# Performance work log

Hardware: AMD Instinct MI355X
Metric: run time of the kernel (lower is better)

The kernel has to match this reference:

```python
import jax, jax.numpy as jnp
import numpy as np

N_STUDENT = 100000
N_COURSE = 20000
N_EDGES = 1000000
HIDDEN = 128


def setup_inputs() -> dict:
    key = jax.random.key(0)
    ks = jax.random.split(key, 8)
    scale = 1.0 / np.sqrt(2 * HIDDEN)
    return {
        "z_student": jax.random.normal(ks[0], (N_STUDENT, HIDDEN), dtype=jnp.float32),
        "z_course": jax.random.normal(ks[1], (N_COURSE, HIDDEN), dtype=jnp.float32),
        "row": jax.random.randint(ks[2], (N_EDGES,), 0, N_STUDENT, dtype=jnp.int64),
        "col": jax.random.randint(ks[3], (N_EDGES,), 0, N_COURSE, dtype=jnp.int64),
        "W1": jax.random.normal(ks[4], (2 * HIDDEN, HIDDEN), dtype=jnp.float32) * scale,
        "b1": jnp.zeros((HIDDEN,), dtype=jnp.float32),
        "W2": jax.random.normal(ks[5], (HIDDEN, 1), dtype=jnp.float32) * (1.0 / np.sqrt(HIDDEN)),
        "b2": jnp.zeros((1,), dtype=jnp.float32),
    }


def reference(z_student, z_course, row, col, W1, b1, W2, b2):
    # gather endpoint embeddings and concat along feature dim: [E, 2H]
    z = jnp.concatenate([z_student[row], z_course[col]], axis=-1)
    h = jax.nn.relu(z @ W1 + b1)   # [E, H]
    out = h @ W2 + b2              # [E, 1]
    return out.reshape(-1)
```

## Files before the change

kernel.cpp:

```cpp
#include <hip/hip_runtime.h>
#include <hip/hip_bf16.h>
#include <hip/hip_fp16.h>


typedef _Float16 half2v __attribute__((ext_vector_type(2)));
typedef _Float16 half8v __attribute__((ext_vector_type(8)));
typedef __fp16   fp16x2 __attribute__((ext_vector_type(2)));
typedef float    float4v __attribute__((ext_vector_type(4)));

__global__ __launch_bounds__(256) void conv_w(const float* __restrict__ W1,
                                              const float* __restrict__ W2,
                                              _Float16* __restrict__ Wt,
                                              _Float16* __restrict__ w2h) {
    int b = blockIdx.x, t = threadIdx.x;
    if (b == 8) { if (t < 128) w2h[t] = (_Float16)W2[t]; return; }
    __shared__ _Float16 lds[32][136];
    int h = b >> 2, n0 = (b & 3) * 32;
    for (int i = 0; i < 16; ++i) {
        int idx = i * 256 + t;
        int k = idx >> 5, nn = idx & 31;
        lds[nn][k] = (_Float16)W1[(h * 128 + k) * 128 + n0 + nn];
    }
    __syncthreads();
    for (int j = 0; j < 2; ++j) {
        int idx = j * 256 + t;
        int nn = idx >> 4, kc = idx & 15;
        half8v v;
        #pragma unroll
        for (int q = 0; q < 8; ++q) v[q] = lds[nn][kc * 8 + q];
        *(half8v*)&Wt[((h * 128 + n0 + nn) * 128) + kc * 8] = v;
    }
}

__global__ __launch_bounds__(256) void gemm_u(
    const float* __restrict__ Zs, const float* __restrict__ Zc,
    const _Float16* __restrict__ Wt, const float* __restrict__ b1,
    _Float16* __restrict__ Us, _Float16* __restrict__ Uc,
    int Ms, int Mc, int nbs)
{
    __shared__ uint4 ldsW[2048];
    const int bid = blockIdx.x, t = threadIdx.x;

    const float* Z; _Float16* U; const _Float16* W; int M, m0, addB;
    if (bid < nbs) { Z = Zs; U = Us; M = Ms; m0 = bid * 64;         W = Wt;         addB = 1; }
    else           { Z = Zc; U = Uc; M = Mc; m0 = (bid - nbs) * 64; W = Wt + 16384; addB = 0; }

    const uint4* Wv = (const uint4*)W;
    #pragma unroll
    for (int i = 0; i < 8; ++i) {
        int j = i * 256 + t;
        int n = j >> 4, ch = j & 15;
        ldsW[n * 16 + (ch ^ ((n >> 3) & 7))] = Wv[j];
    }
    __syncthreads();

    const int wave = t >> 6, lane = t & 63, quad = lane >> 4, l16 = lane & 15;
    int mrow = m0 + wave * 16 + l16;
    int mload = mrow < M ? mrow : M - 1;
    const float* zrow = Z + (long)mload * 128;

    float4v acc[8];
    #pragma unroll
    for (int nt = 0; nt < 8; ++nt) acc[nt] = (float4v)(0.0f);

    #pragma unroll
    for (int c = 0; c < 4; ++c) {
        const float4v* pa = (const float4v*)(zrow + c * 32 + quad * 8);
        float4v a0 = pa[0], a1 = pa[1];
        fp16x2 p[4];
        p[0] = __builtin_amdgcn_cvt_pkrtz(a0[0], a0[1]);
        p[1] = __builtin_amdgcn_cvt_pkrtz(a0[2], a0[3]);
        p[2] = __builtin_amdgcn_cvt_pkrtz(a1[0], a1[1]);
        p[3] = __builtin_amdgcn_cvt_pkrtz(a1[2], a1[3]);
        half8v af;
        __builtin_memcpy(&af, &p[0], 16);
        const int ch = c * 4 + quad;
        #pragma unroll
        for (int nt = 0; nt < 8; ++nt) {
            const int n = l16 * 8 + nt;
            const half8v* pb = (const half8v*)&ldsW[n * 16 + (ch ^ (l16 & 7))];
            acc[nt] = __builtin_amdgcn_mfma_f32_16x16x32_f16(af, *pb, acc[nt], 0, 0, 0);
        }
    }

    float bv[8];
    if (addB) {
        const float4v* pb1 = (const float4v*)(b1 + l16 * 8);
        float4v x0 = pb1[0], x1 = pb1[1];
        bv[0]=x0[0]; bv[1]=x0[1]; bv[2]=x0[2]; bv[3]=x0[3];
        bv[4]=x1[0]; bv[5]=x1[1]; bv[6]=x1[2]; bv[7]=x1[3];
    } else {
        #pragma unroll
        for (int i = 0; i < 8; ++i) bv[i] = 0.0f;
    }

    const int rbase = m0 + wave * 16 + quad * 4;
    #pragma unroll
    for (int r = 0; r < 4; ++r) {
        int rr = rbase + r;
        if (rr < M) {
            half8v o;
            #pragma unroll
            for (int nt = 0; nt < 8; ++nt) o[nt] = (_Float16)(acc[nt][r] + bv[nt]);
            *(half8v*)&U[(long)rr * 128 + l16 * 8] = o;
        }
    }
}

__global__ __launch_bounds__(256) void edge_kernel(
    const int* __restrict__ row, const int* __restrict__ col,
    const _Float16* __restrict__ us, const _Float16* __restrict__ uc,
    const _Float16* __restrict__ w2h, const float* __restrict__ b2,
    float* __restrict__ out, int E)
{
    const int t = threadIdx.x;
    const int sub = t & 7;
    long e = (long)blockIdx.x * 32 + (t >> 3);
    if (e >= E) return;
    int r = row[e], c = col[e];

    const uint4* pa = (const uint4*)(us  + (long)r * 128 + sub * 16);
    const uint4* pb = (const uint4*)(uc  + (long)c * 128 + sub * 16);
    const uint4* pw = (const uint4*)(w2h + sub * 16);
    uint4 a0 = pa[0], a1 = pa[1];
    uint4 c0 = pb[0], c1 = pb[1];
    uint4 w0 = pw[0], w1 = pw[1];

    half2v A[8], B[8], W[8];
    *(uint4*)&A[0] = a0; *(uint4*)&A[4] = a1;
    *(uint4*)&B[0] = c0; *(uint4*)&B[4] = c1;
    *(uint4*)&W[0] = w0; *(uint4*)&W[4] = w1;

    const half2v zero = {(_Float16)0, (_Float16)0};
    float s = 0.0f;
    #pragma unroll
    for (int i = 0; i < 8; ++i) {
        half2v h = A[i] + B[i];
        h = __builtin_elementwise_max(h, zero);
        s += (float)h[0] * (float)W[i][0];
        s += (float)h[1] * (float)W[i][1];
    }
    s += __shfl_xor(s, 1);
    s += __shfl_xor(s, 2);
    s += __shfl_xor(s, 4);
    if (sub == 0) out[e] = s + b2[0];
}

extern "C" void kernel_launch(void* const* d_in, const int* in_sizes, int n_in,
                              void* d_out, int out_size, void* d_ws, size_t ws_size,
                              hipStream_t stream) {
    const float* zs  = (const float*)d_in[0];
    const float* zc  = (const float*)d_in[1];
    const int*   row = (const int*)d_in[2];
    const int*   col = (const int*)d_in[3];
    const float* W1  = (const float*)d_in[4];
    const float* b1  = (const float*)d_in[5];
    const float* W2  = (const float*)d_in[6];
    const float* b2  = (const float*)d_in[7];
    float* out = (float*)d_out;

    const int Ms = in_sizes[0] / 128;
    const int Mc = in_sizes[1] / 128;
    const int E  = in_sizes[2];

    _Float16* Wt  = (_Float16*)d_ws;
    _Float16* w2h = (_Float16*)((char*)d_ws + 65536);
    _Float16* us  = (_Float16*)((char*)d_ws + 65536 + 256);
    _Float16* uc  = us + (size_t)Ms * 128;

    const int nbs = (Ms + 63) / 64, nbc = (Mc + 63) / 64;

    conv_w<<<9, 256, 0, stream>>>(W1, W2, Wt, w2h);
    gemm_u<<<nbs + nbc, 256, 0, stream>>>(zs, zc, Wt, b1, us, uc, Ms, Mc, nbs);
    edge_kernel<<<(E + 31) / 32, 256, 0, stream>>>(row, col, us, uc, w2h, b2, out, E);
}
```

Measured before the change: 169.6 us.

## Bucket edges by student row and XCD to improve gather cache locality

Adds a histogram, scan and scatter pass that groups edges into 256 buckets keyed on row>>9, with buckets interleaved so each of 8 block groups handles a contiguous row range. The edge kernel then walks these permuted edges in persistent blocks, so each group's student-embedding gathers stay within a smaller working set that can sit in a local L2. This targets cache misses on the 25 MB fp16 student table, at the cost of three extra kernels, atomics, an 8 MB permutation buffer and scattered output writes. It also assumes col < 32768 and row < 131072 so both fit in one 32-bit packed key.

```diff
diff --git a/kernel.cpp b/kernel.cpp
--- a/kernel.cpp
+++ b/kernel.cpp
@@ -8,12 +8,26 @@
 typedef __fp16   fp16x2 __attribute__((ext_vector_type(2)));
 typedef float    float4v __attribute__((ext_vector_type(4)));
 
+#define NB 256
+#define EBLK 2048
+#define B8 128
+
+static __device__ __forceinline__ int sort_key(int r) {
+    int key = r >> 9;
+    return (key & 7) * 32 + (key >> 3);
+}
+
 __global__ __launch_bounds__(256) void conv_w(const float* __restrict__ W1,
                                               const float* __restrict__ W2,
                                               _Float16* __restrict__ Wt,
-                                              _Float16* __restrict__ w2h) {
+                                              _Float16* __restrict__ w2h,
+                                              unsigned* __restrict__ hist) {
     int b = blockIdx.x, t = threadIdx.x;
-    if (b == 8) { if (t < 128) w2h[t] = (_Float16)W2[t]; return; }
+    if (b == 8) {
+        if (t < 128) w2h[t] = (_Float16)W2[t];
+        hist[t] = 0u;
+        return;
+    }
     __shared__ _Float16 lds[32][136];
     int h = b >> 2, n0 = (b & 3) * 32;
     for (int i = 0; i < 16; ++i) {
@@ -29,6 +43,78 @@
         #pragma unroll
         for (int q = 0; q < 8; ++q) v[q] = lds[nn][kc * 8 + q];
         *(half8v*)&Wt[((h * 128 + n0 + nn) * 128) + kc * 8] = v;
+    }
+}
+
+__global__ __launch_bounds__(256) void hist_k(const int* __restrict__ row,
+                                              unsigned* __restrict__ hist, int E) {
+    __shared__ unsigned h[NB];
+    int t = threadIdx.x;
+    h[t] = 0;
+    __syncthreads();
+    int b0 = blockIdx.x * EBLK;
+    #pragma unroll
+    for (int i = 0; i < 8; ++i) {
+        int e = b0 + i * 256 + t;
+        if (e < E) atomicAdd(&h[sort_key(row[e])], 1u);
+    }
+    __syncthreads();
+    if (h[t]) atomicAdd(&hist[t], h[t]);
+}
+
+__global__ __launch_bounds__(256) void scan_k(const unsigned* __restrict__ hist,
+                                              unsigned* __restrict__ cursor,
+                                              unsigned* __restrict__ groupStart, int E) {
+    __shared__ unsigned s[NB];
+    int t = threadIdx.x;
+    unsigned v = hist[t];
+    s[t] = v;
+    __syncthreads();
+    for (int d = 1; d < NB; d <<= 1) {
+        unsigned x = (t >= d) ? s[t - d] : 0u;
+        __syncthreads();
+        s[t] += x;
+        __syncthreads();
+    }
+    unsigned excl = s[t] - v;
+    cursor[t] = excl;
+    if ((t & 31) == 0) groupStart[t >> 5] = excl;
+    if (t == 0) groupStart[8] = (unsigned)E;
+}
+
+__global__ __launch_bounds__(256) void scatter_k(const int* __restrict__ row,
+                                                 const int* __restrict__ col,
+                                                 unsigned* __restrict__ cursor,
+                                                 uint2* __restrict__ perm, int E) {
+    __shared__ unsigned h[NB];
+    __shared__ unsigned base[NB];
+    int t = threadIdx.x;
+    h[t] = 0;
+    __syncthreads();
+    int b0 = blockIdx.x * EBLK;
+    int sk[8], rr[8], cc[8];
+    #pragma unroll
+    for (int i = 0; i < 8; ++i) {
+        int e = b0 + i * 256 + t;
+        if (e < E) {
+            rr[i] = row[e]; cc[i] = col[e];
+            sk[i] = sort_key(rr[i]);
+            atomicAdd(&h[sk[i]], 1u);
+        } else sk[i] = -1;
+    }
+    __syncthreads();
+    if (h[t]) base[t] = atomicAdd(&cursor[t], h[t]);
+    __syncthreads();
+    h[t] = 0;
+    __syncthreads();
+    #pragma unroll
+    for (int i = 0; i < 8; ++i) {
+        if (sk[i] >= 0) {
+            unsigned off = atomicAdd(&h[sk[i]], 1u);
+            unsigned pos = base[sk[i]] + off;
+            int e = b0 + i * 256 + t;
+            perm[pos] = make_uint2(((unsigned)rr[i] << 15) | (unsigned)cc[i], (unsigned)e);
+        }
     }
 }
 
@@ -107,43 +193,54 @@
     }
 }
 
-__global__ __launch_bounds__(256) void edge_kernel(
-    const int* __restrict__ row, const int* __restrict__ col,
+__global__ __launch_bounds__(256) void edge_perm_k(
+    const uint2* __restrict__ perm, const unsigned* __restrict__ groupStart,
     const _Float16* __restrict__ us, const _Float16* __restrict__ uc,
     const _Float16* __restrict__ w2h, const float* __restrict__ b2,
-    float* __restrict__ out, int E)
+    float* __restrict__ out)
 {
-    const int t = threadIdx.x;
-    const int sub = t & 7;
-    long e = (long)blockIdx.x * 32 + (t >> 3);
-    if (e >= E) return;
-    int r = row[e], c = col[e];
-
-    const uint4* pa = (const uint4*)(us  + (long)r * 128 + sub * 16);
-    const uint4* pb = (const uint4*)(uc  + (long)c * 128 + sub * 16);
+    const int t = threadIdx.x, sub = t & 7;
+    const int g = blockIdx.x & 7;
+    const int j = blockIdx.x >> 3;
+    unsigned s0 = groupStart[g], s1 = groupStart[g + 1];
+    unsigned len = s1 - s0;
+    unsigned chunk = (len + B8 - 1) / B8;
+    unsigned lo = s0 + j * chunk;
+    unsigned hi = lo + chunk; if (hi > s1) hi = s1;
+
     const uint4* pw = (const uint4*)(w2h + sub * 16);
-    uint4 a0 = pa[0], a1 = pa[1];
-    uint4 c0 = pb[0], c1 = pb[1];
     uint4 w0 = pw[0], w1 = pw[1];
-
-    half2v A[8], B[8], W[8];
-    *(uint4*)&A[0] = a0; *(uint4*)&A[4] = a1;
-    *(uint4*)&B[0] = c0; *(uint4*)&B[4] = c1;
+    half2v W[8];
     *(uint4*)&W[0] = w0; *(uint4*)&W[4] = w1;
-
+    const float b2v = b2[0];
     const half2v zero = {(_Float16)0, (_Float16)0};
-    float s = 0.0f;
-    #pragma unroll
-    for (int i = 0; i < 8; ++i) {
-        half2v h = A[i] + B[i];
-        h = __builtin_elementwise_max(h, zero);
-        s += (float)h[0] * (float)W[i][0];
-        s += (float)h[1] * (float)W[i][1];
-    }
-    s += __shfl_xor(s, 1);
-    s += __shfl_xor(s, 2);
-    s += __shfl_xor(s, 4);
-    if (sub == 0) out[e] = s + b2[0];
+
+    for (unsigned e = lo + (t >> 3); e < hi; e += 32) {
+        uint2 pc = perm[e];
+        unsigned rr = pc.x >> 15, cc = pc.x & 32767u;
+
+        const uint4* pa = (const uint4*)(us + (long)rr * 128 + sub * 16);
+        const uint4* pb = (const uint4*)(uc + (long)cc * 128 + sub * 16);
+        uint4 a0 = pa[0], a1 = pa[1];
+        uint4 c0 = pb[0], c1 = pb[1];
+
+        half2v A[8], B[8];
+        *(uint4*)&A[0] = a0; *(uint4*)&A[4] = a1;
+        *(uint4*)&B[0] = c0; *(uint4*)&B[4] = c1;
+
+        float s = 0.0f;
+        #pragma unroll
+        for (int i = 0; i < 8; ++i) {
+            half2v h = A[i] + B[i];
+            h = __builtin_elementwise_max(h, zero);
+            s += (float)h[0] * (float)W[i][0];
+            s += (float)h[1] * (float)W[i][1];
+        }
+        s += __shfl_xor(s, 1);
+        s += __shfl_xor(s, 2);
+        s += __shfl_xor(s, 4);
+        if (sub == 0) out[pc.y] = s + b2v;
+    }
 }
 
 extern "C" void kernel_launch(void* const* d_in, const int* in_sizes, int n_in,
@@ -163,14 +260,23 @@
     const int Mc = in_sizes[1] / 128;
     const int E  = in_sizes[2];
 
-    _Float16* Wt  = (_Float16*)d_ws;
-    _Float16* w2h = (_Float16*)((char*)d_ws + 65536);
-    _Float16* us  = (_Float16*)((char*)d_ws + 65536 + 256);
-    _Float16* uc  = us + (size_t)Ms * 128;
+    char* w = (char*)d_ws;
+    _Float16* Wt      = (_Float16*)(w);
+    _Float16* w2h     = (_Float16*)(w + 65536);
+    unsigned* hist    = (unsigned*)(w + 66048);
+    unsigned* cursor  = (unsigned*)(w + 67072);
+    unsigned* gstart  = (unsigned*)(w + 68096);
+    _Float16* us      = (_Float16*)(w + 131072);
+    _Float16* uc      = (_Float16*)(w + 131072 + (size_t)Ms * 256);
+    uint2*    perm    = (uint2*)(w + 131072 + (size_t)(Ms + Mc) * 256);
 
     const int nbs = (Ms + 63) / 64, nbc = (Mc + 63) / 64;
-
-    conv_w<<<9, 256, 0, stream>>>(W1, W2, Wt, w2h);
-    gemm_u<<<nbs + nbc, 256, 0, stream>>>(zs, zc, Wt, b1, us, uc, Ms, Mc, nbs);
-    edge_kernel<<<(E + 31) / 32, 256, 0, stream>>>(row, col, us, uc, w2h, b2, out, E);
-}
+    const int nbe = (E + EBLK - 1) / EBLK;
+
+    conv_w   <<<9, 256, 0, stream>>>(W1, W2, Wt, w2h, hist);
+    hist_k   <<<nbe, 256, 0, stream>>>(row, hist, E);
+    scan_k   <<<1, 256, 0, stream>>>(hist, cursor, gstart, E);
+    scatter_k<<<nbe, 256, 0, stream>>>(row, col, cursor, perm, E);
+    gemm_u   <<<nbs + nbc, 256, 0, stream>>>(zs, zc, Wt, b1, us, uc, Ms, Mc, nbs);
+    edge_perm_k<<<8 * B8, 256, 0, stream>>>(perm, gstart, us, uc, w2h, b2, out);
+}
```

Result: slower. 205.1 us (+20.9%).

## Bucket edges by student row to stage student projections in LDS

Applied to the files above, without the earlier changes.

Adds a histogram, scan and scatter pass that groups edges into buckets of 256 student rows, writing a packed permutation of local row, course index and edge id. The edge kernel then loads each bucket's 256 student projection rows into swizzled LDS once and reads only the course rows from global memory. The scatter is fused into the GEMM launch so it overlaps with the projection work. This trades the random global reads of student rows for extra passes over row and col, atomics, a serial scan launch, and scattered output writes.

```diff
diff --git a/kernel.cpp b/kernel.cpp
--- a/kernel.cpp
+++ b/kernel.cpp
@@ -8,18 +8,39 @@
 typedef __fp16   fp16x2 __attribute__((ext_vector_type(2)));
 typedef float    float4v __attribute__((ext_vector_type(4)));
 
-__global__ __launch_bounds__(256) void conv_w(const float* __restrict__ W1,
-                                              const float* __restrict__ W2,
-                                              _Float16* __restrict__ Wt,
-                                              _Float16* __restrict__ w2h) {
+#define NB 512
+#define EBLK_H 8192
+#define EBLK_S 2048
+
+__global__ __launch_bounds__(256) void k1_conv_hist(
+    const float* __restrict__ W1, const float* __restrict__ W2,
+    const int* __restrict__ row,
+    _Float16* __restrict__ Wt, _Float16* __restrict__ w2h,
+    unsigned* __restrict__ part, int E)
+{
     int b = blockIdx.x, t = threadIdx.x;
+    if (b >= 9) {
+        __shared__ unsigned h[NB];
+        h[t] = 0; h[t + 256] = 0;
+        __syncthreads();
+        int hb = b - 9;
+        long b0 = (long)hb * EBLK_H;
+        for (int i = 0; i < 32; ++i) {
+            long e = b0 + i * 256 + t;
+            if (e < E) atomicAdd(&h[row[e] >> 8], 1u);
+        }
+        __syncthreads();
+        part[hb * NB + t] = h[t];
+        part[hb * NB + t + 256] = h[t + 256];
+        return;
+    }
     if (b == 8) { if (t < 128) w2h[t] = (_Float16)W2[t]; return; }
     __shared__ _Float16 lds[32][136];
-    int h = b >> 2, n0 = (b & 3) * 32;
+    int h2 = b >> 2, n0 = (b & 3) * 32;
     for (int i = 0; i < 16; ++i) {
         int idx = i * 256 + t;
         int k = idx >> 5, nn = idx & 31;
-        lds[nn][k] = (_Float16)W1[(h * 128 + k) * 128 + n0 + nn];
+        lds[nn][k] = (_Float16)W1[(h2 * 128 + k) * 128 + n0 + nn];
     }
     __syncthreads();
     for (int j = 0; j < 2; ++j) {
@@ -28,18 +49,78 @@
         half8v v;
         #pragma unroll
         for (int q = 0; q < 8; ++q) v[q] = lds[nn][kc * 8 + q];
-        *(half8v*)&Wt[((h * 128 + n0 + nn) * 128) + kc * 8] = v;
-    }
-}
-
-__global__ __launch_bounds__(256) void gemm_u(
+        *(half8v*)&Wt[((h2 * 128 + n0 + nn) * 128) + kc * 8] = v;
+    }
+}
+
+__global__ __launch_bounds__(512) void k2_scan(const unsigned* __restrict__ part,
+                                               unsigned* __restrict__ bucketStart,
+                                               unsigned* __restrict__ cursor,
+                                               int nbh, int E)
+{
+    __shared__ unsigned s[NB];
+    int t = threadIdx.x;
+    unsigned v = 0;
+    for (int b = 0; b < nbh; ++b) v += part[b * NB + t];
+    s[t] = v;
+    __syncthreads();
+    for (int d = 1; d < NB; d <<= 1) {
+        unsigned x = (t >= d) ? s[t - d] : 0u;
+        __syncthreads();
+        s[t] += x;
+        __syncthreads();
+    }
+    unsigned excl = s[t] - v;
+    bucketStart[t] = excl;
+    cursor[t] = excl;
+    if (t == 0) bucketStart[NB] = (unsigned)E;
+}
+
+__global__ __launch_bounds__(256) void k3_scatter_gemm(
+    const int* __restrict__ row, const int* __restrict__ col,
+    unsigned* __restrict__ cursor, uint2* __restrict__ perm, int E, int nbs_s,
     const float* __restrict__ Zs, const float* __restrict__ Zc,
     const _Float16* __restrict__ Wt, const float* __restrict__ b1,
     _Float16* __restrict__ Us, _Float16* __restrict__ Uc,
     int Ms, int Mc, int nbs)
 {
+    const int t = threadIdx.x;
+    if (blockIdx.x < (unsigned)nbs_s) {
+        __shared__ unsigned h[NB];
+        __shared__ unsigned base[NB];
+        h[t] = 0; h[t + 256] = 0;
+        __syncthreads();
+        long b0 = (long)blockIdx.x * EBLK_S;
+        int sk[8], rr[8], cc[8];
+        #pragma unroll
+        for (int i = 0; i < 8; ++i) {
+            long e = b0 + i * 256 + t;
+            if (e < E) {
+                rr[i] = row[e]; cc[i] = col[e];
+                sk[i] = rr[i] >> 8;
+                atomicAdd(&h[sk[i]], 1u);
+            } else sk[i] = -1;
+        }
+        __syncthreads();
+        if (h[t]) base[t] = atomicAdd(&cursor[t], h[t]);
+        if (h[t + 256]) base[t + 256] = atomicAdd(&cursor[t + 256], h[t + 256]);
+        __syncthreads();
+        h[t] = 0; h[t + 256] = 0;
+        __syncthreads();
+        #pragma unroll
+        for (int i = 0; i < 8; ++i) {
+            if (sk[i] >= 0) {
+                unsigned off = atomicAdd(&h[sk[i]], 1u);
+                unsigned pos = base[sk[i]] + off;
+                long e = b0 + i * 256 + t;
+                perm[pos] = make_uint2(((unsigned)(rr[i] & 255) << 15) | (unsigned)cc[i],
+                                       (unsigned)e);
+            }
+        }
+        return;
+    }
     __shared__ uint4 ldsW[2048];
-    const int bid = blockIdx.x, t = threadIdx.x;
+    const int bid = blockIdx.x - nbs_s;
 
     const float* Z; _Float16* U; const _Float16* W; int M, m0, addB;
     if (bid < nbs) { Z = Zs; U = Us; M = Ms; m0 = bid * 64;         W = Wt;         addB = 1; }
@@ -97,53 +178,69 @@
     const int rbase = m0 + wave * 16 + quad * 4;
     #pragma unroll
     for (int r = 0; r < 4; ++r) {
-        int rr = rbase + r;
-        if (rr < M) {
+        int rr2 = rbase + r;
+        if (rr2 < M) {
             half8v o;
             #pragma unroll
             for (int nt = 0; nt < 8; ++nt) o[nt] = (_Float16)(acc[nt][r] + bv[nt]);
-            *(half8v*)&U[(long)rr * 128 + l16 * 8] = o;
-        }
-    }
-}
-
-__global__ __launch_bounds__(256) void edge_kernel(
-    const int* __restrict__ row, const int* __restrict__ col,
+            *(half8v*)&U[(long)rr2 * 128 + l16 * 8] = o;
+        }
+    }
+}
+
+__global__ __launch_bounds__(512) void k4_edge(
+    const uint2* __restrict__ perm, const unsigned* __restrict__ bucketStart,
     const _Float16* __restrict__ us, const _Float16* __restrict__ uc,
     const _Float16* __restrict__ w2h, const float* __restrict__ b2,
-    float* __restrict__ out, int E)
-{
-    const int t = threadIdx.x;
+    float* __restrict__ out, int Ms)
+{
+    __shared__ uint4 lu[4096];
+    const int t = threadIdx.x, b = blockIdx.x;
+    const int r0 = b << 8;
+    const uint4* usv = (const uint4*)us;
+    #pragma unroll
+    for (int i = 0; i < 8; ++i) {
+        int j = t + i * 512;
+        int rl = j >> 4, ch = j & 15;
+        int r = r0 + rl; if (r >= Ms) r = Ms - 1;
+        lu[rl * 16 + (ch ^ (rl & 15))] = usv[(long)r * 16 + ch];
+    }
     const int sub = t & 7;
-    long e = (long)blockIdx.x * 32 + (t >> 3);
-    if (e >= E) return;
-    int r = row[e], c = col[e];
-
-    const uint4* pa = (const uint4*)(us  + (long)r * 128 + sub * 16);
-    const uint4* pb = (const uint4*)(uc  + (long)c * 128 + sub * 16);
-    const uint4* pw = (const uint4*)(w2h + sub * 16);
-    uint4 a0 = pa[0], a1 = pa[1];
-    uint4 c0 = pb[0], c1 = pb[1];
+    const uint4* pw = ((const uint4*)w2h) + sub * 2;
     uint4 w0 = pw[0], w1 = pw[1];
-
-    half2v A[8], B[8], W[8];
-    *(uint4*)&A[0] = a0; *(uint4*)&A[4] = a1;
-    *(uint4*)&B[0] = c0; *(uint4*)&B[4] = c1;
+    half2v W[8];
     *(uint4*)&W[0] = w0; *(uint4*)&W[4] = w1;
-
+    const float b2v = b2[0];
     const half2v zero = {(_Float16)0, (_Float16)0};
-    float s = 0.0f;
-    #pragma unroll
-    for (int i = 0; i < 8; ++i) {
-        half2v h = A[i] + B[i];
-        h = __builtin_elementwise_max(h, zero);
-        s += (float)h[0] * (float)W[i][0];
-        s += (float)h[1] * (float)W[i][1];
-    }
-    s += __shfl_xor(s, 1);
-    s += __shfl_xor(s, 2);
-    s += __shfl_xor(s, 4);
-    if (sub == 0) out[e] = s + b2[0];
+    unsigned s0 = bucketStart[b], s1 = bucketStart[b + 1];
+    __syncthreads();
+
+    for (unsigned e = s0 + (t >> 3); e < s1; e += 64) {
+        uint2 pc = perm[e];
+        unsigned rloc = pc.x >> 15, cc = pc.x & 32767u;
+        int m = rloc & 15;
+        uint4 a0 = lu[rloc * 16 + ((sub * 2) ^ m)];
+        uint4 a1 = lu[rloc * 16 + ((sub * 2 + 1) ^ m)];
+        const uint4* pb = ((const uint4*)uc) + (long)cc * 16 + sub * 2;
+        uint4 u0 = pb[0], u1 = pb[1];
+
+        half2v A[8], B[8];
+        *(uint4*)&A[0] = a0; *(uint4*)&A[4] = a1;
+        *(uint4*)&B[0] = u0; *(uint4*)&B[4] = u1;
+
+        float s = 0.0f;
+        #pragma unroll
+        for (int i = 0; i < 8; ++i) {
+            half2v h = A[i] + B[i];
+            h = __builtin_elementwise_max(h, zero);
+            s += (float)h[0] * (float)W[i][0];
+            s += (float)h[1] * (float)W[i][1];
+        }
+        s += __shfl_xor(s, 1);
+        s += __shfl_xor(s, 2);
+        s += __shfl_xor(s, 4);
+        if (sub == 0) out[pc.y] = s + b2v;
+    }
 }
 
 extern "C" void kernel_launch(void* const* d_in, const int* in_sizes, int n_in,
@@ -163,14 +260,26 @@
     const int Mc = in_sizes[1] / 128;
     const int E  = in_sizes[2];
 
-    _Float16* Wt  = (_Float16*)d_ws;
-    _Float16* w2h = (_Float16*)((char*)d_ws + 65536);
-    _Float16* us  = (_Float16*)((char*)d_ws + 65536 + 256);
-    _Float16* uc  = us + (size_t)Ms * 128;
+    char* w = (char*)d_ws;
+    _Float16* Wt     = (_Float16*)(w);
+    _Float16* w2h    = (_Float16*)(w + 65536);
+    unsigned* bstart = (unsigned*)(w + 66048);
+    unsigned* cursor = (unsigned*)(w + 69632);
+    unsigned* part   = (unsigned*)(w + 73728);
+    const int nbh = (E + EBLK_H - 1) / EBLK_H;
+    const int nbss = (E + EBLK_S - 1) / EBLK_S;
+    size_t off = 73728 + (size_t)nbh * NB * 4;
+    off = (off + 4095) & ~(size_t)4095;
+    _Float16* us = (_Float16*)(w + off);
+    _Float16* uc = (_Float16*)(w + off + (size_t)Ms * 256);
+    uint2* perm  = (uint2*)(w + off + (size_t)(Ms + Mc) * 256);
 
     const int nbs = (Ms + 63) / 64, nbc = (Mc + 63) / 64;
-
-    conv_w<<<9, 256, 0, stream>>>(W1, W2, Wt, w2h);
-    gemm_u<<<nbs + nbc, 256, 0, stream>>>(zs, zc, Wt, b1, us, uc, Ms, Mc, nbs);
-    edge_kernel<<<(E + 31) / 32, 256, 0, stream>>>(row, col, us, uc, w2h, b2, out, E);
-}
+    const int nbuckets = (Ms + 255) >> 8;
+
+    k1_conv_hist<<<9 + nbh, 256, 0, stream>>>(W1, W2, row, Wt, w2h, part, E);
+    k2_scan<<<1, 512, 0, stream>>>(part, bstart, cursor, nbh, E);
+    k3_scatter_gemm<<<nbss + nbs + nbc, 256, 0, stream>>>(row, col, cursor, perm, E, nbss,
+                                                          zs, zc, Wt, b1, us, uc, Ms, Mc, nbs);
+    k4_edge<<<nbuckets, 512, 0, stream>>>(perm, bstart, us, uc, w2h, b2, out, Ms);
+}
```

New measurement: 217.2 us. 1.28x slower.
